# Performance work log

Measured on AMD Instinct MI355X. Metric: run time of the kernel, lower is better.

## Reference

```python
import jax, jax.numpy as jnp
import numpy as np

B, S, K, D, V = 256, 50, 20, 128, 100000


def setup_inputs() -> dict:
    key = jax.random.key(0)
    ks = jax.random.split(key, 8)
    items = jax.random.randint(ks[0], (B, S, K), 0, V)
    basket_len = jax.random.randint(ks[1], (B, S), 1, K + 1)
    lengths = jnp.sort(jax.random.randint(ks[2], (B,), 1, S + 1))[::-1]
    lengths = lengths.at[0].set(S)  # pack/pad round-trip keeps full seq_len
    encode = jax.random.uniform(ks[3], (V, D), minval=-0.1, maxval=0.1)  # init_weight()
    std = 1.0 / np.sqrt(D)
    w_ih = jax.random.uniform(ks[4], (3 * D, D), minval=-std, maxval=std)
    w_hh = jax.random.uniform(ks[5], (3 * D, D), minval=-std, maxval=std)
    b_ih = jax.random.uniform(ks[6], (3 * D,), minval=-std, maxval=std)
    b_hh = jax.random.uniform(ks[7], (3 * D,), minval=-std, maxval=std)
    h0 = jnp.zeros((1, B, D), dtype=jnp.float32)  # init_hidden (GRU)
    return {"items": items, "basket_len": basket_len, "lengths": lengths,
            "encode": encode, "w_ih": w_ih, "w_hh": w_hh,
            "b_ih": b_ih, "b_hh": b_hh, "h0": h0}


def _basket_pool(encode, items, basket_len, lengths):
    # fused ragged gather + masked mean over basket dim: [B,S,K,D] -> [B,S,D]
    emb = encode[items]
    bmask = (jnp.arange(K)[None, None, :] < basket_len[..., None]).astype(emb.dtype)
    pooled = (emb * bmask[..., None]).sum(axis=2) / basket_len[..., None].astype(emb.dtype)
    smask = (jnp.arange(S)[None, :] < lengths[:, None]).astype(emb.dtype)
    return pooled * smask[..., None], smask


def _gru(xs, smask, w_ih, w_hh, b_ih, b_hh, h0):
    # xs: [B,S,D] -> scan over time; packed-sequence semantics via mask
    xs_t = jnp.swapaxes(xs, 0, 1)          # [S,B,D]
    ms_t = jnp.swapaxes(smask, 0, 1)       # [S,B]

    def step(h, inp):
        x_t, m = inp
        gx = x_t @ w_ih.T + b_ih           # [B,3D]
        gh = h @ w_hh.T + b_hh
        r = jax.nn.sigmoid(gx[:, :D] + gh[:, :D])
        z = jax.nn.sigmoid(gx[:, D:2 * D] + gh[:, D:2 * D])
        n = jnp.tanh(gx[:, 2 * D:] + r * gh[:, 2 * D:])
        hn = (1.0 - z) * n + z * h
        m = m[:, None]
        h_next = jnp.where(m > 0, hn, h)   # hold state past user's length
        y = jnp.where(m > 0, hn, jnp.zeros_like(hn))  # pad_packed zeros
        return h_next, y

    h_last, ys = jax.lax.scan(step, h0[0], (xs_t, ms_t))
    return jnp.swapaxes(ys, 0, 1), h_last[None]  # [B,S,D], [1,B,D]


def reference(items, basket_len, lengths, encode, w_ih, w_hh, b_ih, b_hh, h0):
    pooled, smask = _basket_pool(encode, items, basket_len, lengths)
    dynamic_user, h_u = _gru(pooled, smask, w_ih, w_hh, b_ih, b_hh, h0)
    return dynamic_user, h_u
```

## Files before the change

kernel.cpp:

```cpp
#include <hip/hip_runtime.h>
#include <math.h>

#define B_ 256
#define S_ 50
#define K_ 20
#define D_ 128
#define G3 384
#define M_  (B_ * S_)
#define GROWS 16
#define KT 4

typedef __attribute__((ext_vector_type(8))) short bf16x8;
typedef __attribute__((ext_vector_type(4))) float f32x4;

__device__ inline unsigned short bf16_rne(float f) {
    unsigned u = __float_as_uint(f);
    return (unsigned short)((u + 0x7fffu + ((u >> 16) & 1u)) >> 16);
}
__device__ inline float fsig(float x) {
    return __builtin_amdgcn_rcpf(1.f + __expf(-x));
}
__device__ inline float ftanh(float x) {
    float t = __expf(-2.f * fabsf(x));
    float r = (1.f - t) * __builtin_amdgcn_rcpf(1.f + t);
    return x >= 0.f ? r : -r;
}

#define WG_SYNC_LDS() do { \
    __builtin_amdgcn_sched_barrier(0); \
    asm volatile("s_waitcnt lgkmcnt(0)" ::: "memory"); \
    __builtin_amdgcn_s_barrier(); \
    __builtin_amdgcn_sched_barrier(0); \
} while (0)

__global__ __launch_bounds__(256) void pool_kernel(
    const int* __restrict__ items, const int* __restrict__ basket_len,
    const int* __restrict__ lengths, const float* __restrict__ encode,
    unsigned short* __restrict__ pooled_bf)
{
    const int tid  = threadIdx.x;
    const int pair = tid >> 7;
    const int d    = tid & 127;
    const int m    = blockIdx.x * 2 + pair;
    const int b    = m / S_;
    const int s    = m % S_;
    const int len  = lengths[b];

    float p = 0.f;
    if (s < len) {
        const int  blen = basket_len[m];
        const int* it   = items + m * K_;
        #pragma unroll 4
        for (int k = 0; k < blen; ++k)
            p += encode[(long)it[k] * D_ + d];
        p /= (float)blen;
    }
    pooled_bf[m * D_ + d] = bf16_rne(p);
}

__global__ __launch_bounds__(256) void wih_cvt_kernel(
    const float* __restrict__ w_ih, unsigned short* __restrict__ wih_bf)
{
    int i = blockIdx.x * 256 + threadIdx.x;
    if (i < G3 * D_) wih_bf[i] = bf16_rne(w_ih[i]);
}

__global__ __launch_bounds__(256) void gx_gemm_mfma(
    const unsigned short* __restrict__ pooled_bf,
    const unsigned short* __restrict__ wih_bf,
    const float* __restrict__ b_ih, const float* __restrict__ b_hh,
    float* __restrict__ gx)
{
    __shared__ unsigned short Al[128 * 128];
    __shared__ unsigned short Bl[128 * 128];

    const int tid  = threadIdx.x;
    const int bm   = blockIdx.x % 100;
    const int bn   = blockIdx.x / 100;
    const int m0   = bm * 128;
    const int n0   = bn * 128;
    const int lane = tid & 63;
    const int wv   = tid >> 6;
    const int frow = lane & 15;
    const int fhi  = lane >> 4;
    const int mh   = (wv & 1) * 64;
    const int nh   = (wv >> 1) * 64;

    #pragma unroll
    for (int i = 0; i < 8; ++i) {
        int idx = tid + i * 256;
        int row = idx >> 4, c16 = idx & 15;
        int dst = (row * 256 + c16 * 16) ^ ((row & 7) << 4);
        *(bf16x8*)((char*)Al + dst) =
            *(const bf16x8*)(pooled_bf + (long)(m0 + row) * D_ + c16 * 8);
        *(bf16x8*)((char*)Bl + dst) =
            *(const bf16x8*)(wih_bf + (long)(n0 + row) * D_ + c16 * 8);
    }
    __syncthreads();

    bf16x8 af[4][KT], bfr[4][KT];
    #pragma unroll
    for (int t = 0; t < 4; ++t) {
        #pragma unroll
        for (int kt = 0; kt < KT; ++kt) {
            int ra = mh + t * 16 + frow;
            int oa = (ra * 256 + kt * 64 + fhi * 16) ^ ((ra & 7) << 4);
            af[t][kt] = *(const bf16x8*)((const char*)Al + oa);
            int rb = nh + t * 16 + frow;
            int ob = (rb * 256 + kt * 64 + fhi * 16) ^ ((rb & 7) << 4);
            bfr[t][kt] = *(const bf16x8*)((const char*)Bl + ob);
        }
    }

    f32x4 acc[4][4];
    #pragma unroll
    for (int mt = 0; mt < 4; ++mt)
        #pragma unroll
        for (int nt = 0; nt < 4; ++nt) {
            f32x4 c = {0.f, 0.f, 0.f, 0.f};
            #pragma unroll
            for (int kt = 0; kt < KT; ++kt)
                c = __builtin_amdgcn_mfma_f32_16x16x32_bf16(af[mt][kt], bfr[nt][kt], c, 0, 0, 0);
            acc[mt][nt] = c;
        }

    float bias[4];
    #pragma unroll
    for (int nt = 0; nt < 4; ++nt) {
        int n = n0 + nh + nt * 16 + frow;
        bias[nt] = b_ih[n] + (n < 2 * D_ ? b_hh[n] : 0.f);
    }

    #pragma unroll
    for (int mt = 0; mt < 4; ++mt) {
        #pragma unroll
        for (int nt = 0; nt < 4; ++nt) {
            int n = n0 + nh + nt * 16 + frow;
            #pragma unroll
            for (int r = 0; r < 4; ++r) {
                int row = m0 + mh + mt * 16 + fhi * 4 + r;
                gx[(long)row * G3 + n] = acc[mt][nt][r] + bias[nt];
            }
        }
    }
}

__global__ __launch_bounds__(512, 1) void gru_mfma_kernel(
    const int* __restrict__ lengths, const float* __restrict__ w_hh,
    const float* __restrict__ b_hh, const float* __restrict__ h0,
    const float* __restrict__ gx, float* __restrict__ out)
{
    const int b0   = blockIdx.x * GROWS;
    const int tid  = threadIdx.x;
    const int lane = tid & 63;
    const int wv   = tid >> 6;
    const int frow = lane & 15;
    const int fhi  = lane >> 4;
    const int dim  = wv * 16 + frow;

    __shared__ unsigned short hb[2][GROWS * D_];

    bf16x8 wf[3][KT];
    #pragma unroll
    for (int g = 0; g < 3; ++g) {
        #pragma unroll
        for (int kt = 0; kt < KT; ++kt) {
            const float* wp = w_hh + (g * D_ + dim) * D_ + kt * 32 + fhi * 8;
            bf16x8 v;
            #pragma unroll
            for (int j = 0; j < 8; ++j) v[j] = (short)bf16_rne(wp[j]);
            wf[g][kt] = v;
        }
    }

    const float bhn_s = b_hh[2 * D_ + dim];

    int   mylen[4];
    float hp[4];
    #pragma unroll
    for (int r = 0; r < 4; ++r) {
        int row = fhi * 4 + r;
        mylen[r] = lengths[b0 + row];
        hp[r]    = h0[(long)(b0 + row) * D_ + dim];
        int wb = (row * 256 + dim * 2) ^ ((row & 7) << 4);
        *(unsigned short*)((char*)hb[0] + wb) = bf16_rne(hp[r]);
    }
    const int lenmax = lengths[b0];
    __syncthreads();

    float* ys = out;
    float* hu = out + (long)B_ * S_ * D_;

    const long gxrow[4] = {
        (long)(b0 + fhi * 4 + 0) * S_, (long)(b0 + fhi * 4 + 1) * S_,
        (long)(b0 + fhi * 4 + 2) * S_, (long)(b0 + fhi * 4 + 3) * S_ };

    #define GSTEP(s, CUR, NXT, PP) { \
        const int sn = ((s) + 1 < lenmax) ? (s) + 1 : lenmax - 1; \
        _Pragma("unroll") \
        for (int g = 0; g < 3; ++g) \
            _Pragma("unroll") \
            for (int r = 0; r < 4; ++r) \
                NXT[g][r] = gx[(gxrow[r] + sn) * G3 + g * 128 + dim]; \
        bf16x8 ah[KT]; \
        _Pragma("unroll") \
        for (int kt = 0; kt < KT; ++kt) { \
            int ab = (frow * 256 + kt * 64 + fhi * 16) ^ ((frow & 7) << 4); \
            ah[kt] = *(const bf16x8*)((const char*)hb[PP] + ab); \
        } \
        f32x4 cr = {0.f,0.f,0.f,0.f}, cz = {0.f,0.f,0.f,0.f}, cn = {0.f,0.f,0.f,0.f}; \
        _Pragma("unroll") \
        for (int kt = 0; kt < KT; ++kt) { \
            cr = __builtin_amdgcn_mfma_f32_16x16x32_bf16(ah[kt], wf[0][kt], cr, 0, 0, 0); \
            cz = __builtin_amdgcn_mfma_f32_16x16x32_bf16(ah[kt], wf[1][kt], cz, 0, 0, 0); \
            cn = __builtin_amdgcn_mfma_f32_16x16x32_bf16(ah[kt], wf[2][kt], cn, 0, 0, 0); \
        } \
        _Pragma("unroll") \
        for (int r = 0; r < 4; ++r) { \
            const int row = fhi * 4 + r; \
            const bool act = (s) < mylen[r]; \
            float rg = fsig(CUR[0][r] + cr[r]); \
            float zg = fsig(CUR[1][r] + cz[r]); \
            float ng = ftanh(CUR[2][r] + rg * (cn[r] + bhn_s)); \
            float hn = (1.f - zg) * ng + zg * hp[r]; \
            if (act) { \
                ys[(gxrow[r] + (s)) * D_ + dim] = hn; \
                hp[r] = hn; \
            } \
            int wb = (row * 256 + dim * 2) ^ ((row & 7) << 4); \
            *(unsigned short*)((char*)hb[(PP) ^ 1] + wb) = bf16_rne(hp[r]); \
        } \
        WG_SYNC_LDS(); \
    }

    float curA[3][4], curB[3][4];
    #pragma unroll
    for (int g = 0; g < 3; ++g)
        #pragma unroll
        for (int r = 0; r < 4; ++r)
            curA[g][r] = gx[(gxrow[r] + 0) * G3 + g * 128 + dim];

    int s = 0, pp = 0;
    while (s < lenmax) {
        GSTEP(s, curA, curB, pp);
        ++s; pp ^= 1;
        if (s >= lenmax) break;
        GSTEP(s, curB, curA, pp);
        ++s; pp ^= 1;
    }
    #undef GSTEP

    #pragma unroll
    for (int r = 0; r < 4; ++r) {
        const int row = fhi * 4 + r;
        hu[(long)(b0 + row) * D_ + dim] = hp[r];
        for (int t = mylen[r]; t < S_; ++t)
            ys[((long)(b0 + row) * S_ + t) * D_ + dim] = 0.f;
    }
}

extern "C" void kernel_launch(void* const* d_in, const int* in_sizes, int n_in,
                              void* d_out, int out_size, void* d_ws, size_t ws_size,
                              hipStream_t stream) {
    const int*   items      = (const int*)d_in[0];
    const int*   basket_len = (const int*)d_in[1];
    const int*   lengths    = (const int*)d_in[2];
    const float* encode     = (const float*)d_in[3];
    const float* w_ih       = (const float*)d_in[4];
    const float* w_hh       = (const float*)d_in[5];
    const float* b_ih       = (const float*)d_in[6];
    const float* b_hh       = (const float*)d_in[7];
    const float* h0         = (const float*)d_in[8];
    float* out = (float*)d_out;

    float*          gx        = (float*)d_ws;
    unsigned short* pooled_bf = (unsigned short*)(gx + (long)M_ * G3);
    unsigned short* wih_bf    = pooled_bf + (long)M_ * D_;

    pool_kernel<<<M_ / 2, 256, 0, stream>>>(
        items, basket_len, lengths, encode, pooled_bf);
    wih_cvt_kernel<<<(G3 * D_ + 255) / 256, 256, 0, stream>>>(w_ih, wih_bf);
    gx_gemm_mfma<<<300, 256, 0, stream>>>(
        pooled_bf, wih_bf, b_ih, b_hh, gx);
    gru_mfma_kernel<<<B_ / GROWS, 512, 0, stream>>>(
        lengths, w_hh, b_hh, h0, gx, out);
}
```

Baseline: 81.60 us.

## Fuse basket pooling and weight conversion into the input-gate GEMM kernel

Merges the pooling gather, the w_ih bf16 conversion and the gx GEMM into one kernel. Each of 100 blocks pools 128 rows straight into LDS, then loops over the three 128-column gate tiles of w_ih, converting them to bf16 on the fly. This removes two launches and the pooled_bf global round trip. The cost is that the gather-heavy pooling now runs on only 100 blocks with a long serial loop, which cuts parallelism and latency hiding, and w_ih is reconverted in every block.

```diff
diff --git a/kernel.cpp b/kernel.cpp
--- a/kernel.cpp
+++ b/kernel.cpp
@@ -33,52 +33,17 @@
     __builtin_amdgcn_sched_barrier(0); \
 } while (0)
 
-__global__ __launch_bounds__(256) void pool_kernel(
+__global__ __launch_bounds__(256) void pool_gemm_mfma(
     const int* __restrict__ items, const int* __restrict__ basket_len,
     const int* __restrict__ lengths, const float* __restrict__ encode,
-    unsigned short* __restrict__ pooled_bf)
-{
-    const int tid  = threadIdx.x;
-    const int pair = tid >> 7;
-    const int d    = tid & 127;
-    const int m    = blockIdx.x * 2 + pair;
-    const int b    = m / S_;
-    const int s    = m % S_;
-    const int len  = lengths[b];
-
-    float p = 0.f;
-    if (s < len) {
-        const int  blen = basket_len[m];
-        const int* it   = items + m * K_;
-        #pragma unroll 4
-        for (int k = 0; k < blen; ++k)
-            p += encode[(long)it[k] * D_ + d];
-        p /= (float)blen;
-    }
-    pooled_bf[m * D_ + d] = bf16_rne(p);
-}
-
-__global__ __launch_bounds__(256) void wih_cvt_kernel(
-    const float* __restrict__ w_ih, unsigned short* __restrict__ wih_bf)
-{
-    int i = blockIdx.x * 256 + threadIdx.x;
-    if (i < G3 * D_) wih_bf[i] = bf16_rne(w_ih[i]);
-}
-
-__global__ __launch_bounds__(256) void gx_gemm_mfma(
-    const unsigned short* __restrict__ pooled_bf,
-    const unsigned short* __restrict__ wih_bf,
-    const float* __restrict__ b_ih, const float* __restrict__ b_hh,
-    float* __restrict__ gx)
+    const float* __restrict__ w_ih, const float* __restrict__ b_ih,
+    const float* __restrict__ b_hh, float* __restrict__ gx)
 {
     __shared__ unsigned short Al[128 * 128];
     __shared__ unsigned short Bl[128 * 128];
 
     const int tid  = threadIdx.x;
-    const int bm   = blockIdx.x % 100;
-    const int bn   = blockIdx.x / 100;
-    const int m0   = bm * 128;
-    const int n0   = bn * 128;
+    const int m0   = blockIdx.x * 128;
     const int lane = tid & 63;
     const int wv   = tid >> 6;
     const int frow = lane & 15;
@@ -86,19 +51,29 @@
     const int mh   = (wv & 1) * 64;
     const int nh   = (wv >> 1) * 64;
 
-    #pragma unroll
-    for (int i = 0; i < 8; ++i) {
-        int idx = tid + i * 256;
-        int row = idx >> 4, c16 = idx & 15;
-        int dst = (row * 256 + c16 * 16) ^ ((row & 7) << 4);
-        *(bf16x8*)((char*)Al + dst) =
-            *(const bf16x8*)(pooled_bf + (long)(m0 + row) * D_ + c16 * 8);
-        *(bf16x8*)((char*)Bl + dst) =
-            *(const bf16x8*)(wih_bf + (long)(n0 + row) * D_ + c16 * 8);
+    const int pair = tid >> 7;
+    const int d    = tid & 127;
+    for (int rr = 0; rr < 128; rr += 2) {
+        const int row = rr + pair;
+        const int m   = m0 + row;
+        const int b   = m / S_;
+        const int s   = m - b * S_;
+        const int len = lengths[b];
+        float p = 0.f;
+        if (s < len) {
+            const int  blen = basket_len[m];
+            const int* it   = items + m * K_;
+            #pragma unroll 4
+            for (int k = 0; k < blen; ++k)
+                p += encode[(long)it[k] * D_ + d];
+            p /= (float)blen;
+        }
+        const int dst = (row * 256 + d * 2) ^ ((row & 7) << 4);
+        *(unsigned short*)((char*)Al + dst) = bf16_rne(p);
     }
     __syncthreads();
 
-    bf16x8 af[4][KT], bfr[4][KT];
+    bf16x8 af[4][KT];
     #pragma unroll
     for (int t = 0; t < 4; ++t) {
         #pragma unroll
@@ -106,40 +81,56 @@
             int ra = mh + t * 16 + frow;
             int oa = (ra * 256 + kt * 64 + fhi * 16) ^ ((ra & 7) << 4);
             af[t][kt] = *(const bf16x8*)((const char*)Al + oa);
-            int rb = nh + t * 16 + frow;
-            int ob = (rb * 256 + kt * 64 + fhi * 16) ^ ((rb & 7) << 4);
-            bfr[t][kt] = *(const bf16x8*)((const char*)Bl + ob);
-        }
-    }
-
-    f32x4 acc[4][4];
-    #pragma unroll
-    for (int mt = 0; mt < 4; ++mt)
+        }
+    }
+
+    for (int bn = 0; bn < 3; ++bn) {
+        if (bn) __syncthreads();
+        #pragma unroll
+        for (int i = 0; i < 8; ++i) {
+            int idx = tid + i * 256;
+            int row = idx >> 4, c16 = idx & 15;
+            const float* wp = w_ih + (long)(bn * 128 + row) * D_ + c16 * 8;
+            bf16x8 v;
+            #pragma unroll
+            for (int j = 0; j < 8; ++j) v[j] = (short)bf16_rne(wp[j]);
+            int dst = (row * 256 + c16 * 16) ^ ((row & 7) << 4);
+            *(bf16x8*)((char*)Bl + dst) = v;
+        }
+        __syncthreads();
+
+        bf16x8 bfr[4][KT];
+        #pragma unroll
+        for (int t = 0; t < 4; ++t) {
+            #pragma unroll
+            for (int kt = 0; kt < KT; ++kt) {
+                int rb = nh + t * 16 + frow;
+                int ob = (rb * 256 + kt * 64 + fhi * 16) ^ ((rb & 7) << 4);
+                bfr[t][kt] = *(const bf16x8*)((const char*)Bl + ob);
+            }
+        }
+
+        float bias[4];
         #pragma unroll
         for (int nt = 0; nt < 4; ++nt) {
-            f32x4 c = {0.f, 0.f, 0.f, 0.f};
-            #pragma unroll
-            for (int kt = 0; kt < KT; ++kt)
-                c = __builtin_amdgcn_mfma_f32_16x16x32_bf16(af[mt][kt], bfr[nt][kt], c, 0, 0, 0);
-            acc[mt][nt] = c;
-        }
-
-    float bias[4];
-    #pragma unroll
-    for (int nt = 0; nt < 4; ++nt) {
-        int n = n0 + nh + nt * 16 + frow;
-        bias[nt] = b_ih[n] + (n < 2 * D_ ? b_hh[n] : 0.f);
-    }
-
-    #pragma unroll
-    for (int mt = 0; mt < 4; ++mt) {
-        #pragma unroll
-        for (int nt = 0; nt < 4; ++nt) {
-            int n = n0 + nh + nt * 16 + frow;
-            #pragma unroll
-            for (int r = 0; r < 4; ++r) {
-                int row = m0 + mh + mt * 16 + fhi * 4 + r;
-                gx[(long)row * G3 + n] = acc[mt][nt][r] + bias[nt];
+            int n = bn * 128 + nh + nt * 16 + frow;
+            bias[nt] = b_ih[n] + (n < 2 * D_ ? b_hh[n] : 0.f);
+        }
+
+        #pragma unroll
+        for (int mt = 0; mt < 4; ++mt) {
+            #pragma unroll
+            for (int nt = 0; nt < 4; ++nt) {
+                f32x4 c = {0.f, 0.f, 0.f, 0.f};
+                #pragma unroll
+                for (int kt = 0; kt < KT; ++kt)
+                    c = __builtin_amdgcn_mfma_f32_16x16x32_bf16(af[mt][kt], bfr[nt][kt], c, 0, 0, 0);
+                int n = bn * 128 + nh + nt * 16 + frow;
+                #pragma unroll
+                for (int r = 0; r < 4; ++r) {
+                    int row = m0 + mh + mt * 16 + fhi * 4 + r;
+                    gx[(long)row * G3 + n] = c[r] + bias[nt];
+                }
             }
         }
     }
@@ -273,15 +264,10 @@
     const float* h0         = (const float*)d_in[8];
     float* out = (float*)d_out;
 
-    float*          gx        = (float*)d_ws;
-    unsigned short* pooled_bf = (unsigned short*)(gx + (long)M_ * G3);
-    unsigned short* wih_bf    = pooled_bf + (long)M_ * D_;
-
-    pool_kernel<<<M_ / 2, 256, 0, stream>>>(
-        items, basket_len, lengths, encode, pooled_bf);
-    wih_cvt_kernel<<<(G3 * D_ + 255) / 256, 256, 0, stream>>>(w_ih, wih_bf);
-    gx_gemm_mfma<<<300, 256, 0, stream>>>(
-        pooled_bf, wih_bf, b_ih, b_hh, gx);
+    float* gx = (float*)d_ws;
+
+    pool_gemm_mfma<<<100, 256, 0, stream>>>(
+        items, basket_len, lengths, encode, w_ih, b_ih, b_hh, gx);
     gru_mfma_kernel<<<B_ / GROWS, 512, 0, stream>>>(
         lengths, w_hh, b_hh, h0, gx, out);
 }
```

New measurement: 211.4 us. 2.59x slower.
